# Kernel optimization log

Measured on AMD Instinct MI355X. Metric: run time of the kernel, lower is better.

Reference implementation:

```python
import jax, jax.numpy as jnp
import numpy as np

K, D, N, W, OUT = 16, 2, 16384, 256, 1
TW = 0.2  # fixed_transition_width


def setup_inputs() -> dict:
    key = jax.random.key(0)
    ks = jax.random.split(key, 9)
    # 4x4 grid of subdomains over [0,1]^2
    edges = np.linspace(0.0, 1.0, 5).astype(np.float32)
    mins = np.array([[edges[i], edges[j]] for i in range(4) for j in range(4)], np.float32)
    maxs = mins + 0.25

    def init_w(k, shape, fan_in):
        return jax.random.normal(k, shape, jnp.float32) / np.sqrt(fan_in).astype(np.float32)

    return {
        "x": jax.random.uniform(ks[0], (N, D), jnp.float32),
        "W0": init_w(ks[1], (K, D, W), D),
        "b0": jnp.zeros((K, W), jnp.float32),
        "W1": init_w(ks[2], (K, W, W), W),
        "b1": jnp.zeros((K, W), jnp.float32),
        "W2": init_w(ks[3], (K, W, W), W),
        "b2": jnp.zeros((K, W), jnp.float32),
        "W3": init_w(ks[4], (K, W, OUT), W),
        "b3": jnp.zeros((K, OUT), jnp.float32),
        "xmins": jnp.asarray(mins),
        "xmaxs": jnp.asarray(maxs),
    }


def _cosine_window(xmins, xmaxs, wmin, x):
    """Normalized cosine partition-of-unity weights. x:[N,D], xmins/xmaxs:[K,D] -> [N,K]."""
    # smooth ramp 0->1 over [xmin-w, xmin+w] and 1->0 over [xmax-w, xmax+w], per dim
    t_l = jnp.clip((x[None] - (xmins - wmin)[:, None]) / (2.0 * wmin), 0.0, 1.0)  # [K,N,D]
    t_r = jnp.clip(((xmaxs + wmin)[:, None] - x[None]) / (2.0 * wmin), 0.0, 1.0)
    w_raw = jnp.prod(0.25 * (1.0 - jnp.cos(jnp.pi * t_l)) * (1.0 - jnp.cos(jnp.pi * t_r)), axis=-1)  # [K,N]
    w = w_raw / (jnp.sum(w_raw, axis=0, keepdims=True) + 1e-9)
    return w.T  # [N,K]


def reference(x, W0, b0, W1, b1, W2, b2, W3, b3, xmins, xmaxs):
    all_w = _cosine_window(xmins, xmaxs, TW, x)  # [N,K]
    # per-subdomain normalization of x to [-1,1]
    center = (xmins + xmaxs) * 0.5
    scale = jnp.maximum((xmaxs - xmins) * 0.5, 1e-9)
    xn = (x[None] - center[:, None]) / scale[:, None]  # [K,N,D]
    # batched small MLPs (one per subdomain), tanh hidden activations
    h = jnp.tanh(jnp.einsum('knd,kdw->knw', xn, W0) + b0[:, None])
    h = jnp.tanh(jnp.einsum('knw,kwv->knv', h, W1) + b1[:, None])
    h = jnp.tanh(jnp.einsum('knw,kwv->knv', h, W2) + b2[:, None])
    sub = jnp.einsum('knw,kwo->kno', h, W3) + b3[:, None]  # [K,N,OUT]
    # window-weighted combine; ansatz is identity in the NN output
    return jnp.einsum('nk,kno->no', all_w, sub)  # [N,OUT]
```

## Files before the change

kernel.cpp:

```cpp
#include <hip/hip_runtime.h>
#include <stdint.h>

#define TWF 0.2f
#define NPTS 16384

typedef __attribute__((ext_vector_type(8))) short short8;
typedef __attribute__((ext_vector_type(4))) float floatx4;

__device__ __forceinline__ short f2bf(float f){
  unsigned u = __float_as_uint(f);
  u += 0x7fff + ((u >> 16) & 1);
  return (short)(u >> 16);
}
__device__ __forceinline__ float bf2f(short s){
  return __uint_as_float(((unsigned)(unsigned short)s) << 16);
}
__device__ __forceinline__ float fast_tanh(float x){
  float e = __builtin_amdgcn_exp2f(x * 2.885390082f);
  float r = __builtin_amdgcn_rcpf(e + 1.f);
  return fmaf(-2.f, r, 1.f);
}
__device__ __forceinline__ float cospi_t(float t){
  return __builtin_amdgcn_cosf(t * 0.5f);
}
__device__ __forceinline__ unsigned cvt_pk_bf16(float lo, float hi){
  unsigned r;
  asm("v_cvt_pk_bf16_f32 %0, %1, %2" : "=v"(r) : "v"(lo), "v"(hi));
  return r;
}

#define WS_W      0
#define WS_REC    (4u<<20)
#define WS_CNT    (8u<<20)

struct SMem {
  short lds_h[64 * 256];
  float s_xn[64 * 2];
  float s_win[64];
  int   s_pidx[64];
  float s_w3[256];
  float s_w0[512];
  int   s_stb[257];
  int   s_c[256];
};

__global__ __launch_bounds__(256) void fbpinn_p0(
    const float* __restrict__ W1, const float* __restrict__ W2,
    const float* __restrict__ x,  const float* __restrict__ xmins,
    const float* __restrict__ xmaxs, short* __restrict__ dst,
    int* __restrict__ cnt, floatx4* __restrict__ rec, float* __restrict__ out)
{
  __shared__ int s_wrt[16];
  const int bid = blockIdx.x, t = threadIdx.x;
  int gid = bid * 256 + t;
  {
    int lane = gid & 63; int rest = gid >> 6;
    int jt = rest & 15; rest >>= 4;
    int ks = rest & 7;  rest >>= 3;
    int k  = rest & 15; int mat = rest >> 4;
    const float* W = mat ? W2 : W1;
    int j   = jt * 16 + (lane & 15);
    int kk0 = ks * 32 + (lane >> 4) * 8;
    short8 v;
    #pragma unroll
    for (int jj = 0; jj < 8; jj++)
      v[jj] = f2bf(W[k * 65536 + (kk0 + jj) * 256 + j]);
    *(short8*)(dst + (size_t)gid * 8) = v;
  }
  if (gid < NPTS) out[gid] = 0.f;

  if ((bid & 3) != 0) return;
  int L  = bid >> 2;
  int k  = L & 15, ch = L >> 4;
  int cb = ch * 1024;
  int lane = t & 63, wave = t >> 6;

  float cx  = (xmins[k * 2 + 0] + xmaxs[k * 2 + 0]) * 0.5f;
  float cy  = (xmins[k * 2 + 1] + xmaxs[k * 2 + 1]) * 0.5f;
  float sxi = 1.f / fmaxf((xmaxs[k * 2 + 0] - xmins[k * 2 + 0]) * 0.5f, 1e-9f);
  float syi = 1.f / fmaxf((xmaxs[k * 2 + 1] - xmins[k * 2 + 1]) * 0.5f, 1e-9f);

  float pxr[4], pyr[4], sum[4], wk[4];
  #pragma unroll
  for (int r = 0; r < 4; r++){
    int p = cb + r * 256 + t;
    float2 xy = *(const float2*)&x[p * 2];
    pxr[r] = xy.x; pyr[r] = xy.y; sum[r] = 0.f; wk[r] = 0.f;
  }
  #pragma unroll
  for (int kk = 0; kk < 16; kk++){
    float mnx = xmins[kk * 2 + 0], mny = xmins[kk * 2 + 1];
    float mxx = xmaxs[kk * 2 + 0], mxy = xmaxs[kk * 2 + 1];
    #pragma unroll
    for (int r = 0; r < 4; r++){
      float tlx = fminf(fmaxf((pxr[r] - (mnx - TWF)) * (1.f/(2.f*TWF)), 0.f), 1.f);
      float trx = fminf(fmaxf(((mxx + TWF) - pxr[r]) * (1.f/(2.f*TWF)), 0.f), 1.f);
      float tly = fminf(fmaxf((pyr[r] - (mny - TWF)) * (1.f/(2.f*TWF)), 0.f), 1.f);
      float tr2 = fminf(fmaxf(((mxy + TWF) - pyr[r]) * (1.f/(2.f*TWF)), 0.f), 1.f);
      float wx = 0.25f * (1.f - cospi_t(tlx)) * (1.f - cospi_t(trx));
      float wy = 0.25f * (1.f - cospi_t(tly)) * (1.f - cospi_t(tr2));
      float w  = wx * wy;
      sum[r] += w;
      if (kk == k) wk[r] = w;
    }
  }
  bool act[4]; float wn[4], xa[4], xb[4];
  unsigned long long msk[4]; int wtot[4];
  #pragma unroll
  for (int r = 0; r < 4; r++){
    float inv = 1.f / (sum[r] + 1e-9f);
    act[r] = wk[r] > 0.f;
    wn[r]  = wk[r] * inv;
    xa[r]  = (pxr[r] - cx) * sxi;
    xb[r]  = (pyr[r] - cy) * syi;
    msk[r] = __ballot(act[r]);
    wtot[r] = (int)__popcll(msk[r]);
  }
  if (lane == 0){
    #pragma unroll
    for (int r = 0; r < 4; r++) s_wrt[wave * 4 + r] = wtot[r];
  }
  __syncthreads();
  int wavebase = 0, blocktot = 0;
  #pragma unroll
  for (int w = 0; w < 4; w++){
    int ws_ = s_wrt[w*4+0] + s_wrt[w*4+1] + s_wrt[w*4+2] + s_wrt[w*4+3];
    blocktot += ws_;
    wavebase += (w < wave) ? ws_ : 0;
  }
  if (t == 0) cnt[k * 16 + ch] = blocktot;
  int rb = 0;
  #pragma unroll
  for (int r = 0; r < 4; r++){
    if (act[r]){
      int pos = wavebase + rb + (int)__popcll(msk[r] & ((1ull << lane) - 1ull));
      int p = cb + r * 256 + t;
      rec[k * NPTS + cb + pos] = (floatx4){xa[r], xb[r], wn[r], __int_as_float(p)};
    }
    rb += s_wrt[wave * 4 + r];
  }
}

__device__ __forceinline__ void store_h_packed(
    short* lds_h, const floatx4 (&acc)[4][4], const floatx4 (&bb)[4],
    int wave, int quad, int col){
  #pragma unroll
  for (int rt = 0; rt < 4; rt++){
    const int j0    = (wave * 4 + rt) * 16 + quad * 4;
    const int cbase = j0 >> 3;
    const int off   = j0 & 7;
    #pragma unroll
    for (int ct = 0; ct < 4; ct++){
      const int m = ct * 16 + col;
      float t0 = fast_tanh(acc[rt][ct][0] + bb[rt][0]);
      float t1 = fast_tanh(acc[rt][ct][1] + bb[rt][1]);
      float t2 = fast_tanh(acc[rt][ct][2] + bb[rt][2]);
      float t3 = fast_tanh(acc[rt][ct][3] + bb[rt][3]);
      uint2 v = make_uint2(cvt_pk_bf16(t0, t1), cvt_pk_bf16(t2, t3));
      *(uint2*)&lds_h[m * 256 + ((cbase ^ (m & 7)) << 3) + off] = v;
    }
  }
}

__global__ __launch_bounds__(256, 4) void fbpinn_p1(
    const float* __restrict__ W0, const float* __restrict__ b0,
    const float* __restrict__ b1, const float* __restrict__ b2,
    const float* __restrict__ W3, const float* __restrict__ b3,
    const short* __restrict__ wsw, const int* __restrict__ cnt,
    const floatx4* __restrict__ rec, float* __restrict__ out)
{
  __shared__ SMem sm;
  const int bid  = blockIdx.x, t = threadIdx.x;
  const int lane = t & 63;
  const int wave = t >> 6;
  const int col  = lane & 15;
  const int quad = lane >> 4;

  int* s_scan = (int*)sm.lds_h;
  if (t < 256){ int c = cnt[t]; sm.s_c[t] = c; s_scan[t] = (c + 63) >> 6; }
  __syncthreads();
  for (int off = 1; off < 256; off <<= 1){
    int v = (t >= off) ? s_scan[t - off] : 0;
    __syncthreads();
    s_scan[t] += v;
    __syncthreads();
  }
  if (t < 256) sm.s_stb[t + 1] = s_scan[t];
  if (t == 0)  sm.s_stb[0] = 0;
  __syncthreads();
  const int total = sm.s_stb[256];

  const int xcd    = bid & 7;
  const int nb     = gridDim.x >> 3;
  const int chunkT = (total + 7) >> 3;

  for (int idx = bid >> 3; idx < chunkT; idx += nb){
    const int tile = xcd * chunkT + idx;
    if (tile >= total) break;
    int lo = 0, hi = 256;
    while (hi - lo > 1){
      int mid = (lo + hi) >> 1;
      if (tile >= sm.s_stb[mid]) lo = mid; else hi = mid;
    }
    const int seg = lo, k = seg >> 4, ch = seg & 15;
    const int c     = sm.s_c[seg];
    const int lbase = (tile - sm.s_stb[seg]) * 64;
    const floatx4* rbase = rec + k * NPTS + ch * 1024;

    __syncthreads();

    sm.s_w3[t] = W3[k * 256 + t];
    sm.s_w0[t] = W0[k * 512 + t];
    sm.s_w0[256 + t] = W0[k * 512 + 256 + t];
    if (t < 64){
      int li = lbase + t;
      bool valid = li < c;
      floatx4 rcd = rbase[valid ? li : 0];
      sm.s_pidx[t] = __float_as_int(rcd[3]);
      sm.s_win[t]  = valid ? rcd[2] : 0.f;
      sm.s_xn[t * 2 + 0] = rcd[0];
      sm.s_xn[t * 2 + 1] = rcd[1];
    }
    __syncthreads();

    {
      short8 wfr[4], xfr[4];
      #pragma unroll
      for (int rt = 0; rt < 4; rt++){
        int j = (wave * 4 + rt) * 16 + col;
        short8 a;
        #pragma unroll
        for (int i = 0; i < 8; i++) a[i] = 0;
        a[0] = (quad == 0) ? f2bf(sm.s_w0[j])       : (short)0;
        a[1] = (quad == 0) ? f2bf(sm.s_w0[256 + j]) : (short)0;
        wfr[rt] = a;
      }
      #pragma unroll
      for (int ct = 0; ct < 4; ct++){
        int m = ct * 16 + col;
        short8 b;
        #pragma unroll
        for (int i = 0; i < 8; i++) b[i] = 0;
        b[0] = (quad == 0) ? f2bf(sm.s_xn[m * 2 + 0]) : (short)0;
        b[1] = (quad == 0) ? f2bf(sm.s_xn[m * 2 + 1]) : (short)0;
        xfr[ct] = b;
      }
      floatx4 bb[4];
      #pragma unroll
      for (int rt = 0; rt < 4; rt++)
        bb[rt] = *(const floatx4*)&b0[k * 256 + (wave * 4 + rt) * 16 + quad * 4];
      floatx4 acc[4][4];
      #pragma unroll
      for (int a = 0; a < 4; a++)
        #pragma unroll
        for (int b = 0; b < 4; b++)
          acc[a][b] = (floatx4){0.f, 0.f, 0.f, 0.f};
      #pragma unroll
      for (int rt = 0; rt < 4; rt++)
        #pragma unroll
        for (int ct = 0; ct < 4; ct++)
          acc[rt][ct] = __builtin_amdgcn_mfma_f32_16x16x32_bf16(wfr[rt], xfr[ct], acc[rt][ct], 0, 0, 0);
      store_h_packed(sm.lds_h, acc, bb, wave, quad, col);
      __syncthreads();
    }

    #pragma unroll 1
    for (int layer = 0; layer < 2; layer++){
      const short8* wb = (const short8*)(wsw + (size_t)layer * 1048576)
                         + ((size_t)(k * 8) * 16 + wave * 4) * 64 + lane;
      const float*  bp = layer ? b2 : b1;
      floatx4 bb[4];
      #pragma unroll
      for (int rt = 0; rt < 4; rt++)
        bb[rt] = *(const floatx4*)&bp[k * 256 + (wave * 4 + rt) * 16 + quad * 4];
      floatx4 acc[4][4];
      #pragma unroll
      for (int a = 0; a < 4; a++)
        #pragma unroll
        for (int b = 0; b < 4; b++)
          acc[a][b] = (floatx4){0.f, 0.f, 0.f, 0.f};

      short8 wcur[4];
      #pragma unroll
      for (int rt = 0; rt < 4; rt++) wcur[rt] = wb[rt * 64];

      #pragma unroll
      for (int ks = 0; ks < 8; ks++){
        short8 wnxt[4];
        if (ks < 7){
          #pragma unroll
          for (int rt = 0; rt < 4; rt++)
            wnxt[rt] = wb[(ks + 1) * 1024 + rt * 64];
        }
        short8 hfr[4];
        #pragma unroll
        for (int ct = 0; ct < 4; ct++){
          int m   = ct * 16 + col;
          int pos = (ks * 4 + quad) ^ (m & 7);
          hfr[ct] = *(const short8*)&sm.lds_h[m * 256 + pos * 8];
        }
        #pragma unroll
        for (int rt = 0; rt < 4; rt++)
          #pragma unroll
          for (int ct = 0; ct < 4; ct++)
            acc[rt][ct] = __builtin_amdgcn_mfma_f32_16x16x32_bf16(wcur[rt], hfr[ct], acc[rt][ct], 0, 0, 0);
        if (ks < 7){
          #pragma unroll
          for (int rt = 0; rt < 4; rt++) wcur[rt] = wnxt[rt];
        }
      }
      __syncthreads();

      store_h_packed(sm.lds_h, acc, bb, wave, quad, col);
      __syncthreads();
    }

    {
      int m = t >> 2, q = t & 3;
      float dot = 0.f;
      #pragma unroll
      for (int cc = 0; cc < 8; cc++){
        int ci  = q * 8 + cc;
        int pos = ci ^ (m & 7);
        short8 hv = *(const short8*)&sm.lds_h[m * 256 + pos * 8];
        #pragma unroll
        for (int jj = 0; jj < 8; jj++)
          dot = fmaf(bf2f(hv[jj]), sm.s_w3[ci * 8 + jj], dot);
      }
      dot += __shfl_xor(dot, 1);
      dot += __shfl_xor(dot, 2);
      if (q == 0 && sm.s_win[m] != 0.f)
        atomicAdd(&out[sm.s_pidx[m]], sm.s_win[m] * (dot + b3[k]));
    }
  }
}

extern "C" void kernel_launch(void* const* d_in, const int* in_sizes, int n_in,
                              void* d_out, int out_size, void* d_ws, size_t ws_size,
                              hipStream_t stream){
  const float* x     = (const float*)d_in[0];
  const float* W0    = (const float*)d_in[1];
  const float* b0    = (const float*)d_in[2];
  const float* W1    = (const float*)d_in[3];
  const float* b1    = (const float*)d_in[4];
  const float* W2    = (const float*)d_in[5];
  const float* b2    = (const float*)d_in[6];
  const float* W3    = (const float*)d_in[7];
  const float* b3    = (const float*)d_in[8];
  const float* xmins = (const float*)d_in[9];
  const float* xmaxs = (const float*)d_in[10];
  float* out = (float*)d_out;

  char* ws = (char*)d_ws;
  short*   wsw  = (short*)  (ws + WS_W);
  floatx4* rec  = (floatx4*)(ws + WS_REC);
  int*     cnt  = (int*)    (ws + WS_CNT);

  fbpinn_p0<<<1024, 256, 0, stream>>>(W1, W2, x, xmins, xmaxs,
                                      wsw, cnt, rec, out);
  fbpinn_p1<<<1024, 256, 0, stream>>>(W0, b0, b1, b2, W3, b3,
                                      wsw, cnt, rec, out);
}
```

Measured before the change: 153.6 us.

## Halve MLP point tile, use fixed-slot scheduling, and stage weight conversion through LDS

The per-tile point count in the MLP kernel drops from 64 to 32, which shrinks the LDS footprint so the kernel can run at higher occupancy (launch bounds 7, grid 1792). The prefix-scan and binary-search tile assignment is replaced by fixed 32-point slots per segment, and empty slots are skipped. The weight bf16 swizzle kernel now does coalesced vector loads into a padded LDS tile instead of strided scalar global reads, and runs as a dedicated 256-block section of a smaller grid. In exchange, each loaded weight fragment now feeds fewer MFMAs, so weight reuse per tile is lower, and the fixed slot walk adds iterations that skip empty slots.

```diff
diff --git a/kernel.cpp b/kernel.cpp
--- a/kernel.cpp
+++ b/kernel.cpp
@@ -32,17 +32,6 @@
 #define WS_W      0
 #define WS_REC    (4u<<20)
 #define WS_CNT    (8u<<20)
-
-struct SMem {
-  short lds_h[64 * 256];
-  float s_xn[64 * 2];
-  float s_win[64];
-  int   s_pidx[64];
-  float s_w3[256];
-  float s_w0[512];
-  int   s_stb[257];
-  int   s_c[256];
-};
 
 __global__ __launch_bounds__(256) void fbpinn_p0(
     const float* __restrict__ W1, const float* __restrict__ W2,
@@ -50,30 +39,49 @@
     const float* __restrict__ xmaxs, short* __restrict__ dst,
     int* __restrict__ cnt, floatx4* __restrict__ rec, float* __restrict__ out)
 {
-  __shared__ int s_wrt[16];
+  __shared__ short lds_w[32 * 264];
+  __shared__ int   s_wrt[16];
   const int bid = blockIdx.x, t = threadIdx.x;
-  int gid = bid * 256 + t;
-  {
-    int lane = gid & 63; int rest = gid >> 6;
-    int jt = rest & 15; rest >>= 4;
-    int ks = rest & 7;  rest >>= 3;
-    int k  = rest & 15; int mat = rest >> 4;
+
+  if (bid < 256){
+    int mat = bid >> 7, rem = bid & 127, k = rem >> 3, ks = rem & 7;
     const float* W = mat ? W2 : W1;
-    int j   = jt * 16 + (lane & 15);
-    int kk0 = ks * 32 + (lane >> 4) * 8;
-    short8 v;
-    #pragma unroll
-    for (int jj = 0; jj < 8; jj++)
-      v[jj] = f2bf(W[k * 65536 + (kk0 + jj) * 256 + j]);
-    *(short8*)(dst + (size_t)gid * 8) = v;
-  }
-  if (gid < NPTS) out[gid] = 0.f;
-
-  if ((bid & 3) != 0) return;
-  int L  = bid >> 2;
+    const float* srcRow = W + k * 65536 + (ks * 32) * 256;
+    int r  = t >> 3;
+    int cb = (t & 7) * 32;
+    int cbs = cb ^ (((r >> 3) & 1) << 5);
+    #pragma unroll
+    for (int i = 0; i < 4; i++){
+      floatx4 f0 = *(const floatx4*)(srcRow + r * 256 + cb + i * 8);
+      floatx4 f1 = *(const floatx4*)(srcRow + r * 256 + cb + i * 8 + 4);
+      short8 v;
+      v[0] = f2bf(f0[0]); v[1] = f2bf(f0[1]); v[2] = f2bf(f0[2]); v[3] = f2bf(f0[3]);
+      v[4] = f2bf(f1[0]); v[5] = f2bf(f1[1]); v[6] = f2bf(f1[2]); v[7] = f2bf(f1[3]);
+      *(short8*)&lds_w[r * 264 + cbs + i * 8] = v;
+    }
+    __syncthreads();
+    size_t base = (size_t)mat * 131072 + k * 8192 + ks * 1024;
+    #pragma unroll
+    for (int rr = 0; rr < 4; rr++){
+      int ridx = t + rr * 256;
+      int ln = ridx & 63, jt = ridx >> 6;
+      int j  = jt * 16 + (ln & 15);
+      int q  = ln >> 4;
+      int jx = j ^ ((q & 1) << 5);
+      short8 v;
+      #pragma unroll
+      for (int jj = 0; jj < 8; jj++)
+        v[jj] = lds_w[(q * 8 + jj) * 264 + jx];
+      *(short8*)(dst + (base + ridx) * 8) = v;
+    }
+    return;
+  }
+
+  int L  = bid - 256;
   int k  = L & 15, ch = L >> 4;
   int cb = ch * 1024;
   int lane = t & 63, wave = t >> 6;
+  if (t < 64) out[L * 64 + t] = 0.f;
 
   float cx  = (xmins[k * 2 + 0] + xmaxs[k * 2 + 0]) * 0.5f;
   float cy  = (xmins[k * 2 + 1] + xmaxs[k * 2 + 1]) * 0.5f;
@@ -142,7 +150,7 @@
 }
 
 __device__ __forceinline__ void store_h_packed(
-    short* lds_h, const floatx4 (&acc)[4][4], const floatx4 (&bb)[4],
+    short* lds_h, const floatx4 (&acc)[4][2], const floatx4 (&bb)[4],
     int wave, int quad, int col){
   #pragma unroll
   for (int rt = 0; rt < 4; rt++){
@@ -150,7 +158,7 @@
     const int cbase = j0 >> 3;
     const int off   = j0 & 7;
     #pragma unroll
-    for (int ct = 0; ct < 4; ct++){
+    for (int ct = 0; ct < 2; ct++){
       const int m = ct * 16 + col;
       float t0 = fast_tanh(acc[rt][ct][0] + bb[rt][0]);
       float t1 = fast_tanh(acc[rt][ct][1] + bb[rt][1]);
@@ -162,105 +170,96 @@
   }
 }
 
-__global__ __launch_bounds__(256, 4) void fbpinn_p1(
+__global__ __launch_bounds__(256, 7) void fbpinn_p1(
     const float* __restrict__ W0, const float* __restrict__ b0,
     const float* __restrict__ b1, const float* __restrict__ b2,
     const float* __restrict__ W3, const float* __restrict__ b3,
     const short* __restrict__ wsw, const int* __restrict__ cnt,
     const floatx4* __restrict__ rec, float* __restrict__ out)
 {
-  __shared__ SMem sm;
+  __shared__ short lds_h[32 * 256];
+  __shared__ float s_xn[32 * 2];
+  __shared__ float s_win[32];
+  __shared__ int   s_pidx[32];
+  __shared__ float s_w3[256];
+  __shared__ float s_w0[512];
+  __shared__ int   s_c[256];
+
   const int bid  = blockIdx.x, t = threadIdx.x;
   const int lane = t & 63;
   const int wave = t >> 6;
   const int col  = lane & 15;
   const int quad = lane >> 4;
 
-  int* s_scan = (int*)sm.lds_h;
-  if (t < 256){ int c = cnt[t]; sm.s_c[t] = c; s_scan[t] = (c + 63) >> 6; }
+  if (t < 256) s_c[t] = cnt[t];
   __syncthreads();
-  for (int off = 1; off < 256; off <<= 1){
-    int v = (t >= off) ? s_scan[t - off] : 0;
+
+  const int xcd = bid & 7;
+  const int nb  = gridDim.x >> 3;
+
+  for (int s = bid >> 3; s < 1024; s += nb){
+    const int slot = xcd * 1024 + s;
+    const int seg  = slot >> 5, ti = slot & 31;
+    const int c    = s_c[seg];
+    if (ti * 32 >= c) continue;
+    const int k = seg >> 4, ch = seg & 15;
+    const int lbase = ti * 32;
+    const floatx4* rbase = rec + k * NPTS + ch * 1024;
+
     __syncthreads();
-    s_scan[t] += v;
-    __syncthreads();
-  }
-  if (t < 256) sm.s_stb[t + 1] = s_scan[t];
-  if (t == 0)  sm.s_stb[0] = 0;
-  __syncthreads();
-  const int total = sm.s_stb[256];
-
-  const int xcd    = bid & 7;
-  const int nb     = gridDim.x >> 3;
-  const int chunkT = (total + 7) >> 3;
-
-  for (int idx = bid >> 3; idx < chunkT; idx += nb){
-    const int tile = xcd * chunkT + idx;
-    if (tile >= total) break;
-    int lo = 0, hi = 256;
-    while (hi - lo > 1){
-      int mid = (lo + hi) >> 1;
-      if (tile >= sm.s_stb[mid]) lo = mid; else hi = mid;
-    }
-    const int seg = lo, k = seg >> 4, ch = seg & 15;
-    const int c     = sm.s_c[seg];
-    const int lbase = (tile - sm.s_stb[seg]) * 64;
-    const floatx4* rbase = rec + k * NPTS + ch * 1024;
-
-    __syncthreads();
-
-    sm.s_w3[t] = W3[k * 256 + t];
-    sm.s_w0[t] = W0[k * 512 + t];
-    sm.s_w0[256 + t] = W0[k * 512 + 256 + t];
-    if (t < 64){
+
+    s_w3[t] = W3[k * 256 + t];
+    s_w0[t] = W0[k * 512 + t];
+    s_w0[256 + t] = W0[k * 512 + 256 + t];
+    if (t < 32){
       int li = lbase + t;
       bool valid = li < c;
       floatx4 rcd = rbase[valid ? li : 0];
-      sm.s_pidx[t] = __float_as_int(rcd[3]);
-      sm.s_win[t]  = valid ? rcd[2] : 0.f;
-      sm.s_xn[t * 2 + 0] = rcd[0];
-      sm.s_xn[t * 2 + 1] = rcd[1];
+      s_pidx[t] = __float_as_int(rcd[3]);
+      s_win[t]  = valid ? rcd[2] : 0.f;
+      s_xn[t * 2 + 0] = rcd[0];
+      s_xn[t * 2 + 1] = rcd[1];
     }
     __syncthreads();
 
     {
-      short8 wfr[4], xfr[4];
+      short8 wfr[4], xfr[2];
       #pragma unroll
       for (int rt = 0; rt < 4; rt++){
         int j = (wave * 4 + rt) * 16 + col;
         short8 a;
         #pragma unroll
         for (int i = 0; i < 8; i++) a[i] = 0;
-        a[0] = (quad == 0) ? f2bf(sm.s_w0[j])       : (short)0;
-        a[1] = (quad == 0) ? f2bf(sm.s_w0[256 + j]) : (short)0;
+        a[0] = (quad == 0) ? f2bf(s_w0[j])       : (short)0;
+        a[1] = (quad == 0) ? f2bf(s_w0[256 + j]) : (short)0;
         wfr[rt] = a;
       }
       #pragma unroll
-      for (int ct = 0; ct < 4; ct++){
+      for (int ct = 0; ct < 2; ct++){
         int m = ct * 16 + col;
         short8 b;
         #pragma unroll
         for (int i = 0; i < 8; i++) b[i] = 0;
-        b[0] = (quad == 0) ? f2bf(sm.s_xn[m * 2 + 0]) : (short)0;
-        b[1] = (quad == 0) ? f2bf(sm.s_xn[m * 2 + 1]) : (short)0;
+        b[0] = (quad == 0) ? f2bf(s_xn[m * 2 + 0]) : (short)0;
+        b[1] = (quad == 0) ? f2bf(s_xn[m * 2 + 1]) : (short)0;
         xfr[ct] = b;
       }
       floatx4 bb[4];
       #pragma unroll
       for (int rt = 0; rt < 4; rt++)
         bb[rt] = *(const floatx4*)&b0[k * 256 + (wave * 4 + rt) * 16 + quad * 4];
-      floatx4 acc[4][4];
+      floatx4 acc[4][2];
       #pragma unroll
       for (int a = 0; a < 4; a++)
         #pragma unroll
-        for (int b = 0; b < 4; b++)
+        for (int b = 0; b < 2; b++)
           acc[a][b] = (floatx4){0.f, 0.f, 0.f, 0.f};
       #pragma unroll
       for (int rt = 0; rt < 4; rt++)
         #pragma unroll
-        for (int ct = 0; ct < 4; ct++)
+        for (int ct = 0; ct < 2; ct++)
           acc[rt][ct] = __builtin_amdgcn_mfma_f32_16x16x32_bf16(wfr[rt], xfr[ct], acc[rt][ct], 0, 0, 0);
-      store_h_packed(sm.lds_h, acc, bb, wave, quad, col);
+      store_h_packed(lds_h, acc, bb, wave, quad, col);
       __syncthreads();
     }
 
@@ -273,11 +272,11 @@
       #pragma unroll
       for (int rt = 0; rt < 4; rt++)
         bb[rt] = *(const floatx4*)&bp[k * 256 + (wave * 4 + rt) * 16 + quad * 4];
-      floatx4 acc[4][4];
+      floatx4 acc[4][2];
       #pragma unroll
       for (int a = 0; a < 4; a++)
         #pragma unroll
-        for (int b = 0; b < 4; b++)
+        for (int b = 0; b < 2; b++)
           acc[a][b] = (floatx4){0.f, 0.f, 0.f, 0.f};
 
       short8 wcur[4];
@@ -292,17 +291,17 @@
           for (int rt = 0; rt < 4; rt++)
             wnxt[rt] = wb[(ks + 1) * 1024 + rt * 64];
         }
-        short8 hfr[4];
-        #pragma unroll
-        for (int ct = 0; ct < 4; ct++){
+        short8 hfr[2];
+        #pragma unroll
+        for (int ct = 0; ct < 2; ct++){
           int m   = ct * 16 + col;
           int pos = (ks * 4 + quad) ^ (m & 7);
-          hfr[ct] = *(const short8*)&sm.lds_h[m * 256 + pos * 8];
+          hfr[ct] = *(const short8*)&lds_h[m * 256 + pos * 8];
         }
         #pragma unroll
         for (int rt = 0; rt < 4; rt++)
           #pragma unroll
-          for (int ct = 0; ct < 4; ct++)
+          for (int ct = 0; ct < 2; ct++)
             acc[rt][ct] = __builtin_amdgcn_mfma_f32_16x16x32_bf16(wcur[rt], hfr[ct], acc[rt][ct], 0, 0, 0);
         if (ks < 7){
           #pragma unroll
@@ -311,26 +310,27 @@
       }
       __syncthreads();
 
-      store_h_packed(sm.lds_h, acc, bb, wave, quad, col);
+      store_h_packed(lds_h, acc, bb, wave, quad, col);
       __syncthreads();
     }
 
     {
-      int m = t >> 2, q = t & 3;
+      int m = t >> 3, q = t & 7;
       float dot = 0.f;
       #pragma unroll
-      for (int cc = 0; cc < 8; cc++){
-        int ci  = q * 8 + cc;
+      for (int cc = 0; cc < 4; cc++){
+        int ci  = q * 4 + cc;
         int pos = ci ^ (m & 7);
-        short8 hv = *(const short8*)&sm.lds_h[m * 256 + pos * 8];
+        short8 hv = *(const short8*)&lds_h[m * 256 + pos * 8];
         #pragma unroll
         for (int jj = 0; jj < 8; jj++)
-          dot = fmaf(bf2f(hv[jj]), sm.s_w3[ci * 8 + jj], dot);
+          dot = fmaf(bf2f(hv[jj]), s_w3[ci * 8 + jj], dot);
       }
       dot += __shfl_xor(dot, 1);
       dot += __shfl_xor(dot, 2);
-      if (q == 0 && sm.s_win[m] != 0.f)
-        atomicAdd(&out[sm.s_pidx[m]], sm.s_win[m] * (dot + b3[k]));
+      dot += __shfl_xor(dot, 4);
+      if (q == 0 && s_win[m] != 0.f)
+        atomicAdd(&out[s_pidx[m]], s_win[m] * (dot + b3[k]));
     }
   }
 }
@@ -356,8 +356,8 @@
   floatx4* rec  = (floatx4*)(ws + WS_REC);
   int*     cnt  = (int*)    (ws + WS_CNT);
 
-  fbpinn_p0<<<1024, 256, 0, stream>>>(W1, W2, x, xmins, xmaxs,
+  fbpinn_p0<<<512, 256, 0, stream>>>(W1, W2, x, xmins, xmaxs,
+                                     wsw, cnt, rec, out);
+  fbpinn_p1<<<1792, 256, 0, stream>>>(W0, b0, b1, b2, W3, b3,
                                       wsw, cnt, rec, out);
-  fbpinn_p1<<<1024, 256, 0, stream>>>(W0, b0, b1, b2, W3, b3,
-                                      wsw, cnt, rec, out);
-}
+}
```

After: 208.1 us. 1.35x slower.
